# Kernel tuning notes

Measured on AMD Instinct MI355X. Metric: run time of the kernel, lower is better.

Reference implementation:

```python
import jax, jax.numpy as jnp
import numpy as np

K = 2  # kernel_size == stride, padding=0, dilation=1 -> non-overlapping 2x2x2 blocks


def setup_inputs() -> dict:
    key = jax.random.key(0)
    # (b, c, s, w, h) volumetric batch
    x = jax.random.normal(key, (8, 1, 64, 192, 192), dtype=jnp.float32)
    return {"x": x}


def _extract_blocks(x, k):
    # Faithful to extract_patches_3d with stride==kernel, padding=0, dilation=1:
    # the double unfold + permute + flat view yields rows ordered (b, c, do, ho, wo),
    # each row the flattened k*k*k patch.
    b, c, s, w, h = x.shape
    blk = x.reshape(b, c, s // k, k, w // k, k, h // k, k)
    blk = blk.transpose(0, 1, 2, 4, 6, 3, 5, 7)  # (b,c,do,ho,wo,k,k,k)
    return blk.reshape(-1, k * k * k)  # (N, k^3)


def reference(x):
    b, c, s, w, h = x.shape
    data = _extract_blocks(x, K)            # (N, 8)
    mean = jnp.mean(data, axis=0)           # (8,)
    centered = data - mean
    # torch.svd: data = U S V^T ; jax returns vh = V^T
    _, _, vh = jnp.linalg.svd(centered, full_matrices=False)
    pca_components = vh[:1].T               # (8, n_components=1)
    reduced = centered @ pca_components     # (N, 1)
    out = reduced.reshape(b, c, s // K, w // K, h // K)
    return out, mean, pca_components
```

## Files before the change

kernel.cpp:

```cpp
#include <hip/hip_runtime.h>

constexpr int NB     = 8 * 32 * 96 * 96;
constexpr int NQUAD  = NB / 4;
constexpr int NACC   = 44;
constexpr int GRID_A = 768;
constexpr int TPB    = 256;
constexpr int GRID_P = 768;

__global__ __launch_bounds__(TPB, 4)
void reduce_kernel(const float* __restrict__ x, float* __restrict__ partials,
                   unsigned int* __restrict__ ctr, unsigned int* __restrict__ flag) {
  if (blockIdx.x == 0 && threadIdx.x == 0) { *ctr = 0u; *flag = 0u; }

  float acc[NACC];
#pragma unroll
  for (int i = 0; i < NACC; ++i) acc[i] = 0.0f;

  int t = threadIdx.x;
  int tid = blockIdx.x * TPB + t;
  const int stride = GRID_A * TPB;
  for (int q = tid; q < NQUAD; q += stride) {
    int hq = q % 24;
    int t1 = q / 24;
    int wo = t1 % 96;
    int t2 = t1 / 96;
    int so = t2 % 32;
    int b  = t2 / 32;
    const float* base = x + (((b * 64 + 2 * so) * 192 + 2 * wo) * 192 + 8 * hq);
    float4 a0 = *(const float4*)(base);
    float4 b0 = *(const float4*)(base + 4);
    float4 a1 = *(const float4*)(base + 192);
    float4 b1 = *(const float4*)(base + 196);
    float4 a2 = *(const float4*)(base + 192 * 192);
    float4 b2 = *(const float4*)(base + 192 * 192 + 4);
    float4 a3 = *(const float4*)(base + 192 * 192 + 192);
    float4 b3 = *(const float4*)(base + 192 * 192 + 196);
    float P[4][8] = {
      {a0.x, a0.y, a1.x, a1.y, a2.x, a2.y, a3.x, a3.y},
      {a0.z, a0.w, a1.z, a1.w, a2.z, a2.w, a3.z, a3.w},
      {b0.x, b0.y, b1.x, b1.y, b2.x, b2.y, b3.x, b3.y},
      {b0.z, b0.w, b1.z, b1.w, b2.z, b2.w, b3.z, b3.w}};
#pragma unroll
    for (int a = 0; a < 8; ++a)
      acc[a] += (P[0][a] + P[1][a]) + (P[2][a] + P[3][a]);
    int k = 8;
#pragma unroll
    for (int a = 0; a < 8; ++a)
#pragma unroll
      for (int c = a; c < 8; ++c) {
        float tt = P[0][a] * P[0][c];
        tt += P[1][a] * P[1][c];
        tt += P[2][a] * P[2][c];
        tt += P[3][a] * P[3][c];
        acc[k++] += tt;
      }
  }

#pragma unroll
  for (int i = 0; i < NACC; ++i) {
    float v = acc[i];
    for (int off = 32; off >= 1; off >>= 1) v += __shfl_down(v, off, 64);
    acc[i] = v;
  }
  __shared__ float lds[4][NACC];
  int lane = t & 63;
  int wv   = t >> 6;
  if (lane == 0) {
#pragma unroll
    for (int i = 0; i < NACC; ++i) lds[wv][i] = acc[i];
  }
  __syncthreads();
  if (t < NACC) {
    float s = lds[0][t] + lds[1][t] + lds[2][t] + lds[3][t];
    partials[t * GRID_A + blockIdx.x] = s;
  }
}

__device__ __forceinline__ float rdlane(float x, int lane) {
  return __int_as_float(__builtin_amdgcn_readlane(__float_as_int(x), lane));
}

template <int P, int Q>
__device__ __forceinline__ void jrot(const float (&r)[8], float& ct, float& st) {
  float app = rdlane(r[P], P);
  float aqq = rdlane(r[Q], Q);
  float apq = rdlane(r[Q], P);
  float theta = (aqq - app) * 0.5f * __builtin_amdgcn_rcpf(apq);
  float root  = __builtin_amdgcn_sqrtf(theta * theta + 1.0f);
  float tmag  = __builtin_amdgcn_rcpf(fabsf(theta) + root);
  float tt    = copysignf(tmag, theta);
  float c     = __builtin_amdgcn_rsqf(tt * tt + 1.0f);
  float s     = tt * c;
  bool zero   = (apq == 0.0f);
  ct = zero ? 1.0f : c;
  st = zero ? 0.0f : s;
}

template <int P, int Q>
__device__ __forceinline__ void jcol(float (&r)[8], float (&v)[8], float c, float s) {
  float rp = r[P], rq = r[Q];
  r[P] = c * rp - s * rq;
  r[Q] = s * rp + c * rq;
  float vp = v[P], vq = v[Q];
  v[P] = c * vp - s * vq;
  v[Q] = s * vp + c * vq;
}

template <int P0,int Q0,int P1,int Q1,int P2,int Q2,int P3,int Q3>
__device__ __forceinline__ void jacobi_round(float (&r)[8], float (&v)[8], int i) {
  float c0,s0,c1,s1,c2,s2,c3,s3;
  jrot<P0,Q0>(r, c0, s0);
  jrot<P1,Q1>(r, c1, s1);
  jrot<P2,Q2>(r, c2, s2);
  jrot<P3,Q3>(r, c3, s3);
  jcol<P0,Q0>(r, v, c0, s0);
  jcol<P1,Q1>(r, v, c1, s1);
  jcol<P2,Q2>(r, v, c2, s2);
  jcol<P3,Q3>(r, v, c3, s3);
  float alpha = 1.0f, beta = 0.0f;
  int plane = i;
  if (i == P0) { alpha = c0; beta = -s0; plane = Q0; }
  if (i == Q0) { alpha = c0; beta =  s0; plane = P0; }
  if (i == P1) { alpha = c1; beta = -s1; plane = Q1; }
  if (i == Q1) { alpha = c1; beta =  s1; plane = P1; }
  if (i == P2) { alpha = c2; beta = -s2; plane = Q2; }
  if (i == Q2) { alpha = c2; beta =  s2; plane = P2; }
  if (i == P3) { alpha = c3; beta = -s3; plane = Q3; }
  if (i == Q3) { alpha = c3; beta =  s3; plane = P3; }
  float prow[8];
#pragma unroll
  for (int j = 0; j < 8; ++j) prow[j] = __shfl(r[j], plane, 64);
#pragma unroll
  for (int j = 0; j < 8; ++j) r[j] = alpha * r[j] + beta * prow[j];
}

__global__ __launch_bounds__(TPB, 4)
void project_solve_kernel(const float* __restrict__ x,
                          const float* __restrict__ partials,
                          double* __restrict__ sums_d,
                          unsigned int* __restrict__ ctr,
                          unsigned int* __restrict__ flag,
                          float* __restrict__ res,
                          float* __restrict__ out,
                          float* __restrict__ out_tail) {
  int t = threadIdx.x;

  if (blockIdx.x < NACC) {
    double s = 0.0;
    if (t < GRID_A / 4) {
      float4 u = ((const float4*)(partials + blockIdx.x * GRID_A))[t];
      s = (double)u.x + (double)u.y + (double)u.z + (double)u.w;
    }
    for (int off = 32; off >= 1; off >>= 1) s += __shfl_down(s, off, 64);
    __shared__ double ldsd[4];
    __shared__ bool is_last;
    if ((t & 63) == 0) ldsd[t >> 6] = s;
    __syncthreads();
    if (t == 0) {
      sums_d[blockIdx.x] = ldsd[0] + ldsd[1] + ldsd[2] + ldsd[3];
      __threadfence();
      unsigned int old = atomicAdd(ctr, 1u);
      is_last = (old == (unsigned int)(NACC - 1));
    }
    __syncthreads();
    if (is_last) {
      __threadfence();
      __shared__ double sums[NACC];
      if (t < NACC) sums[t] = sums_d[t];
      __syncthreads();
      if (t < 64) {
        const int i = t & 7;
        const double invN = 1.0 / (double)NB;
        double mean[8];
#pragma unroll
        for (int j = 0; j < 8; ++j) mean[j] = sums[j] * invN;
        double mean_i = mean[0];
#pragma unroll
        for (int k = 1; k < 8; ++k) if (i == k) mean_i = mean[k];
        double rowd[8];
#pragma unroll
        for (int j = 0; j < 8; ++j) {
          int p = i < j ? i : j;
          int q = i < j ? j : i;
          int idx = 8 + p * 8 - (p * (p - 1)) / 2 + (q - p);
          rowd[j] = sums[idx] - (double)NB * mean_i * mean[j];
        }
        double tr = 0.0;
#pragma unroll
        for (int k = 0; k < 8; ++k) tr += __shfl(rowd[k], k, 64);
        double shift = tr * 0.125;

        float r[8], v[8];
#pragma unroll
        for (int j = 0; j < 8; ++j) {
          double d = rowd[j] - (j == i ? shift : 0.0);
          r[j] = (float)(d * (1.0 / 1536.0));
          v[j] = (j == i) ? 1.0f : 0.0f;
        }
#pragma unroll 1
        for (int sweep = 0; sweep < 5; ++sweep) {
          jacobi_round<7,0, 1,6, 2,5, 3,4>(r, v, i);
          jacobi_round<7,1, 2,0, 3,6, 4,5>(r, v, i);
          jacobi_round<7,2, 3,1, 4,0, 5,6>(r, v, i);
          jacobi_round<7,3, 4,2, 5,1, 6,0>(r, v, i);
          jacobi_round<7,4, 5,3, 6,2, 0,1>(r, v, i);
          jacobi_round<7,5, 6,4, 0,3, 1,2>(r, v, i);
          jacobi_round<7,6, 0,5, 1,4, 2,3>(r, v, i);
        }
        float diag[8];
#pragma unroll
        for (int k = 0; k < 8; ++k) diag[k] = rdlane(r[k], k);
        int best = 0; float bd = diag[0];
#pragma unroll
        for (int k = 1; k < 8; ++k) if (diag[k] > bd) { bd = diag[k]; best = k; }
        float vi = v[0];
#pragma unroll
        for (int k = 1; k < 8; ++k) if (best == k) vi = v[k];
        float vec[8];
#pragma unroll
        for (int k = 0; k < 8; ++k) vec[k] = rdlane(vi, k);
        float nrm2 = 0.0f;
#pragma unroll
        for (int k = 0; k < 8; ++k) nrm2 += vec[k] * vec[k];
        float inv = 1.0f / sqrtf(nrm2);
#pragma unroll
        for (int k = 0; k < 8; ++k) vec[k] *= inv;
        int m = 0; float am = fabsf(vec[0]);
#pragma unroll
        for (int k = 1; k < 8; ++k) { float aa = fabsf(vec[k]); if (aa > am) { am = aa; m = k; } }
        float vm = vec[0];
#pragma unroll
        for (int k = 1; k < 8; ++k) if (m == k) vm = vec[k];
        if (vm > 0.0f) {
#pragma unroll
          for (int k = 0; k < 8; ++k) vec[k] = -vec[k];
        }
        double c0d = 0.0;
#pragma unroll
        for (int k = 0; k < 8; ++k) c0d += mean[k] * (double)vec[k];
        float mi = (float)mean[0];
#pragma unroll
        for (int k = 1; k < 8; ++k) if (i == k) mi = (float)mean[k];
        float vl = vec[0];
#pragma unroll
        for (int k = 1; k < 8; ++k) if (i == k) vl = vec[k];
        if (t < 8) {
          res[t]          = vl;
          out_tail[t]     = mi;
          out_tail[8 + t] = vl;
        }
        if (t == 0) res[8] = (float)c0d;
      }
      __syncthreads();
      if (t == 0) {
        __threadfence();
        __hip_atomic_store(flag, 1u, __ATOMIC_RELEASE, __HIP_MEMORY_SCOPE_AGENT);
      }
    }
  }

  __shared__ float s_res[9];
  if (t == 0) {
    while (__hip_atomic_load(flag, __ATOMIC_RELAXED, __HIP_MEMORY_SCOPE_AGENT) == 0u)
      __builtin_amdgcn_s_sleep(8);
  }
  __syncthreads();
  if (t < 9)
    s_res[t] = __hip_atomic_load(&res[t], __ATOMIC_RELAXED, __HIP_MEMORY_SCOPE_AGENT);
  __syncthreads();

  float w0 = s_res[0], w1 = s_res[1], w2 = s_res[2], w3 = s_res[3];
  float w4 = s_res[4], w5 = s_res[5], w6 = s_res[6], w7 = s_res[7];
  float c0 = s_res[8];
  float4* out4 = (float4*)out;
  const int stride = GRID_P * TPB;
  for (int q = blockIdx.x * TPB + t; q < NQUAD; q += stride) {
    int hq = q % 24;
    int t1 = q / 24;
    int wo = t1 % 96;
    int t2 = t1 / 96;
    int so = t2 % 32;
    int b  = t2 / 32;
    const float* base = x + (((b * 64 + 2 * so) * 192 + 2 * wo) * 192 + 8 * hq);
    float4 a0 = *(const float4*)(base);
    float4 b0 = *(const float4*)(base + 4);
    float4 a1 = *(const float4*)(base + 192);
    float4 b1 = *(const float4*)(base + 196);
    float4 a2 = *(const float4*)(base + 192 * 192);
    float4 b2 = *(const float4*)(base + 192 * 192 + 4);
    float4 a3 = *(const float4*)(base + 192 * 192 + 192);
    float4 b3 = *(const float4*)(base + 192 * 192 + 196);
    float o0 = a0.x * w0 + a0.y * w1 + a1.x * w2 + a1.y * w3
             + a2.x * w4 + a2.y * w5 + a3.x * w6 + a3.y * w7 - c0;
    float o1 = a0.z * w0 + a0.w * w1 + a1.z * w2 + a1.w * w3
             + a2.z * w4 + a2.w * w5 + a3.z * w6 + a3.w * w7 - c0;
    float o2 = b0.x * w0 + b0.y * w1 + b1.x * w2 + b1.y * w3
             + b2.x * w4 + b2.y * w5 + b3.x * w6 + b3.y * w7 - c0;
    float o3 = b0.z * w0 + b0.w * w1 + b1.z * w2 + b1.w * w3
             + b2.z * w4 + b2.w * w5 + b3.z * w6 + b3.w * w7 - c0;
    out4[q] = make_float4(o0, o1, o2, o3);
  }
}

extern "C" void kernel_launch(void* const* d_in, const int* in_sizes, int n_in,
                              void* d_out, int out_size, void* d_ws, size_t ws_size,
                              hipStream_t stream) {
  (void)in_sizes; (void)n_in; (void)out_size; (void)ws_size;
  const float* x = (const float*)d_in[0];
  float* out = (float*)d_out;
  float* partials   = (float*)d_ws;
  double* sums_d    = (double*)(partials + NACC * GRID_A);
  float* res        = (float*)(sums_d + NACC);
  unsigned int* ctr = (unsigned int*)(res + 16);
  unsigned int* flg = ctr + 1;

  reduce_kernel<<<GRID_A, TPB, 0, stream>>>(x, partials, ctr, flg);
  project_solve_kernel<<<GRID_P, TPB, 0, stream>>>(x, partials, sums_d, ctr, flg,
                                                   res, out, out + NB);
}
```

Before: 55.26 us.

## Move final partial reduction into reduce kernel, solve eigenproblem redundantly per block

Removes the spin-wait flag handshake in the projection kernel. The last 44 blocks of the reduce kernel now wait on an atomic counter and each folds one accumulator row into sums_d. Every projection block then recomputes the 8x8 Jacobi eigen-solve locally, so no cross-block dependency remains. Also fixes the grid-stride loops at three iterations and adds a memset launch to reset the counter. Trades redundant per-block solve work and a small extra memset for the removal of the serialized global wait.

Measured after the change: 116.7 us. 2.11x slower.

```diff
diff --git a/kernel.cpp b/kernel.cpp
--- a/kernel.cpp
+++ b/kernel.cpp
@@ -6,20 +6,20 @@
 constexpr int GRID_A = 768;
 constexpr int TPB    = 256;
 constexpr int GRID_P = 768;
+constexpr int STRIDE = GRID_A * TPB;
 
 __global__ __launch_bounds__(TPB, 4)
 void reduce_kernel(const float* __restrict__ x, float* __restrict__ partials,
-                   unsigned int* __restrict__ ctr, unsigned int* __restrict__ flag) {
-  if (blockIdx.x == 0 && threadIdx.x == 0) { *ctr = 0u; *flag = 0u; }
-
+                   double* __restrict__ sums_d, unsigned int* __restrict__ ctr) {
   float acc[NACC];
 #pragma unroll
   for (int i = 0; i < NACC; ++i) acc[i] = 0.0f;
 
   int t = threadIdx.x;
   int tid = blockIdx.x * TPB + t;
-  const int stride = GRID_A * TPB;
-  for (int q = tid; q < NQUAD; q += stride) {
+#pragma unroll
+  for (int it = 0; it < 3; ++it) {
+    int q = tid + it * STRIDE;
     int hq = q % 24;
     int t1 = q / 24;
     int wo = t1 % 96;
@@ -74,6 +74,34 @@
     float s = lds[0][t] + lds[1][t] + lds[2][t] + lds[3][t];
     partials[t * GRID_A + blockIdx.x] = s;
   }
+
+  __threadfence();
+  __syncthreads();
+  __shared__ unsigned int oldv;
+  if (t == 0) oldv = atomicAdd(ctr, 1u);
+  __syncthreads();
+  unsigned int old = oldv;
+  if (old < (unsigned int)(GRID_A - NACC)) return;
+  int row = (int)old - (GRID_A - NACC);
+
+  if (t == 0) {
+    while (__hip_atomic_load(ctr, __ATOMIC_RELAXED, __HIP_MEMORY_SCOPE_AGENT)
+           < (unsigned int)GRID_A)
+      __builtin_amdgcn_s_sleep(1);
+  }
+  __syncthreads();
+  __threadfence();
+
+  double s = 0.0;
+  if (t < GRID_A / 4) {
+    float4 u = ((const float4*)(partials + row * GRID_A))[t];
+    s = (double)u.x + (double)u.y + (double)u.z + (double)u.w;
+  }
+  for (int off = 32; off >= 1; off >>= 1) s += __shfl_down(s, off, 64);
+  __shared__ double ldsd[4];
+  if (lane == 0) ldsd[wv] = s;
+  __syncthreads();
+  if (t == 0) sums_d[row] = ldsd[0] + ldsd[1] + ldsd[2] + ldsd[3];
 }
 
 __device__ __forceinline__ float rdlane(float x, int lane) {
@@ -136,145 +164,112 @@
 
 __global__ __launch_bounds__(TPB, 4)
 void project_solve_kernel(const float* __restrict__ x,
-                          const float* __restrict__ partials,
-                          double* __restrict__ sums_d,
-                          unsigned int* __restrict__ ctr,
-                          unsigned int* __restrict__ flag,
-                          float* __restrict__ res,
+                          const double* __restrict__ sums_d,
                           float* __restrict__ out,
                           float* __restrict__ out_tail) {
+  __shared__ double sums[NACC];
+  __shared__ float s_res[9];
   int t = threadIdx.x;
 
-  if (blockIdx.x < NACC) {
-    double s = 0.0;
-    if (t < GRID_A / 4) {
-      float4 u = ((const float4*)(partials + blockIdx.x * GRID_A))[t];
-      s = (double)u.x + (double)u.y + (double)u.z + (double)u.w;
-    }
-    for (int off = 32; off >= 1; off >>= 1) s += __shfl_down(s, off, 64);
-    __shared__ double ldsd[4];
-    __shared__ bool is_last;
-    if ((t & 63) == 0) ldsd[t >> 6] = s;
-    __syncthreads();
-    if (t == 0) {
-      sums_d[blockIdx.x] = ldsd[0] + ldsd[1] + ldsd[2] + ldsd[3];
-      __threadfence();
-      unsigned int old = atomicAdd(ctr, 1u);
-      is_last = (old == (unsigned int)(NACC - 1));
-    }
-    __syncthreads();
-    if (is_last) {
-      __threadfence();
-      __shared__ double sums[NACC];
-      if (t < NACC) sums[t] = sums_d[t];
-      __syncthreads();
-      if (t < 64) {
-        const int i = t & 7;
-        const double invN = 1.0 / (double)NB;
-        double mean[8];
-#pragma unroll
-        for (int j = 0; j < 8; ++j) mean[j] = sums[j] * invN;
-        double mean_i = mean[0];
-#pragma unroll
-        for (int k = 1; k < 8; ++k) if (i == k) mean_i = mean[k];
-        double rowd[8];
-#pragma unroll
-        for (int j = 0; j < 8; ++j) {
-          int p = i < j ? i : j;
-          int q = i < j ? j : i;
-          int idx = 8 + p * 8 - (p * (p - 1)) / 2 + (q - p);
-          rowd[j] = sums[idx] - (double)NB * mean_i * mean[j];
-        }
-        double tr = 0.0;
-#pragma unroll
-        for (int k = 0; k < 8; ++k) tr += __shfl(rowd[k], k, 64);
-        double shift = tr * 0.125;
-
-        float r[8], v[8];
-#pragma unroll
-        for (int j = 0; j < 8; ++j) {
-          double d = rowd[j] - (j == i ? shift : 0.0);
-          r[j] = (float)(d * (1.0 / 1536.0));
-          v[j] = (j == i) ? 1.0f : 0.0f;
-        }
+  if (t < NACC) sums[t] = sums_d[t];
+  __syncthreads();
+
+  if (t < 64) {
+    const int i = t & 7;
+    const double invN = 1.0 / (double)NB;
+    double mean[8];
+#pragma unroll
+    for (int j = 0; j < 8; ++j) mean[j] = sums[j] * invN;
+    double mean_i = mean[0];
+#pragma unroll
+    for (int k = 1; k < 8; ++k) if (i == k) mean_i = mean[k];
+    double rowd[8];
+#pragma unroll
+    for (int j = 0; j < 8; ++j) {
+      int p = i < j ? i : j;
+      int q = i < j ? j : i;
+      int idx = 8 + p * 8 - (p * (p - 1)) / 2 + (q - p);
+      rowd[j] = sums[idx] - (double)NB * mean_i * mean[j];
+    }
+    double tr = 0.0;
+#pragma unroll
+    for (int k = 0; k < 8; ++k) tr += __shfl(rowd[k], k, 64);
+    double shift = tr * 0.125;
+
+    float r[8], v[8];
+#pragma unroll
+    for (int j = 0; j < 8; ++j) {
+      double d = rowd[j] - (j == i ? shift : 0.0);
+      r[j] = (float)(d * (1.0 / 1536.0));
+      v[j] = (j == i) ? 1.0f : 0.0f;
+    }
 #pragma unroll 1
-        for (int sweep = 0; sweep < 5; ++sweep) {
-          jacobi_round<7,0, 1,6, 2,5, 3,4>(r, v, i);
-          jacobi_round<7,1, 2,0, 3,6, 4,5>(r, v, i);
-          jacobi_round<7,2, 3,1, 4,0, 5,6>(r, v, i);
-          jacobi_round<7,3, 4,2, 5,1, 6,0>(r, v, i);
-          jacobi_round<7,4, 5,3, 6,2, 0,1>(r, v, i);
-          jacobi_round<7,5, 6,4, 0,3, 1,2>(r, v, i);
-          jacobi_round<7,6, 0,5, 1,4, 2,3>(r, v, i);
-        }
-        float diag[8];
-#pragma unroll
-        for (int k = 0; k < 8; ++k) diag[k] = rdlane(r[k], k);
-        int best = 0; float bd = diag[0];
-#pragma unroll
-        for (int k = 1; k < 8; ++k) if (diag[k] > bd) { bd = diag[k]; best = k; }
-        float vi = v[0];
-#pragma unroll
-        for (int k = 1; k < 8; ++k) if (best == k) vi = v[k];
-        float vec[8];
-#pragma unroll
-        for (int k = 0; k < 8; ++k) vec[k] = rdlane(vi, k);
-        float nrm2 = 0.0f;
-#pragma unroll
-        for (int k = 0; k < 8; ++k) nrm2 += vec[k] * vec[k];
-        float inv = 1.0f / sqrtf(nrm2);
-#pragma unroll
-        for (int k = 0; k < 8; ++k) vec[k] *= inv;
-        int m = 0; float am = fabsf(vec[0]);
-#pragma unroll
-        for (int k = 1; k < 8; ++k) { float aa = fabsf(vec[k]); if (aa > am) { am = aa; m = k; } }
-        float vm = vec[0];
-#pragma unroll
-        for (int k = 1; k < 8; ++k) if (m == k) vm = vec[k];
-        if (vm > 0.0f) {
-#pragma unroll
-          for (int k = 0; k < 8; ++k) vec[k] = -vec[k];
-        }
-        double c0d = 0.0;
-#pragma unroll
-        for (int k = 0; k < 8; ++k) c0d += mean[k] * (double)vec[k];
-        float mi = (float)mean[0];
-#pragma unroll
-        for (int k = 1; k < 8; ++k) if (i == k) mi = (float)mean[k];
-        float vl = vec[0];
-#pragma unroll
-        for (int k = 1; k < 8; ++k) if (i == k) vl = vec[k];
-        if (t < 8) {
-          res[t]          = vl;
-          out_tail[t]     = mi;
-          out_tail[8 + t] = vl;
-        }
-        if (t == 0) res[8] = (float)c0d;
+    for (int sweep = 0; sweep < 5; ++sweep) {
+      jacobi_round<7,0, 1,6, 2,5, 3,4>(r, v, i);
+      jacobi_round<7,1, 2,0, 3,6, 4,5>(r, v, i);
+      jacobi_round<7,2, 3,1, 4,0, 5,6>(r, v, i);
+      jacobi_round<7,3, 4,2, 5,1, 6,0>(r, v, i);
+      jacobi_round<7,4, 5,3, 6,2, 0,1>(r, v, i);
+      jacobi_round<7,5, 6,4, 0,3, 1,2>(r, v, i);
+      jacobi_round<7,6, 0,5, 1,4, 2,3>(r, v, i);
+    }
+    float diag[8];
+#pragma unroll
+    for (int k = 0; k < 8; ++k) diag[k] = rdlane(r[k], k);
+    int best = 0; float bd = diag[0];
+#pragma unroll
+    for (int k = 1; k < 8; ++k) if (diag[k] > bd) { bd = diag[k]; best = k; }
+    float vi = v[0];
+#pragma unroll
+    for (int k = 1; k < 8; ++k) if (best == k) vi = v[k];
+    float vec[8];
+#pragma unroll
+    for (int k = 0; k < 8; ++k) vec[k] = rdlane(vi, k);
+    float nrm2 = 0.0f;
+#pragma unroll
+    for (int k = 0; k < 8; ++k) nrm2 += vec[k] * vec[k];
+    float inv = 1.0f / sqrtf(nrm2);
+#pragma unroll
+    for (int k = 0; k < 8; ++k) vec[k] *= inv;
+    int m = 0; float am = fabsf(vec[0]);
+#pragma unroll
+    for (int k = 1; k < 8; ++k) { float aa = fabsf(vec[k]); if (aa > am) { am = aa; m = k; } }
+    float vm = vec[0];
+#pragma unroll
+    for (int k = 1; k < 8; ++k) if (m == k) vm = vec[k];
+    if (vm > 0.0f) {
+#pragma unroll
+      for (int k = 0; k < 8; ++k) vec[k] = -vec[k];
+    }
+    double c0d = 0.0;
+#pragma unroll
+    for (int k = 0; k < 8; ++k) c0d += mean[k] * (double)vec[k];
+    float mi = (float)mean[0];
+#pragma unroll
+    for (int k = 1; k < 8; ++k) if (i == k) mi = (float)mean[k];
+    float vl = vec[0];
+#pragma unroll
+    for (int k = 1; k < 8; ++k) if (i == k) vl = vec[k];
+
+    if (t < 8) {
+      s_res[t] = vl;
+      if (blockIdx.x == 0) {
+        out_tail[t]     = mi;
+        out_tail[8 + t] = vl;
       }
-      __syncthreads();
-      if (t == 0) {
-        __threadfence();
-        __hip_atomic_store(flag, 1u, __ATOMIC_RELEASE, __HIP_MEMORY_SCOPE_AGENT);
-      }
-    }
-  }
-
-  __shared__ float s_res[9];
-  if (t == 0) {
-    while (__hip_atomic_load(flag, __ATOMIC_RELAXED, __HIP_MEMORY_SCOPE_AGENT) == 0u)
-      __builtin_amdgcn_s_sleep(8);
-  }
-  __syncthreads();
-  if (t < 9)
-    s_res[t] = __hip_atomic_load(&res[t], __ATOMIC_RELAXED, __HIP_MEMORY_SCOPE_AGENT);
+    }
+    if (t == 0) s_res[8] = (float)c0d;
+  }
   __syncthreads();
 
   float w0 = s_res[0], w1 = s_res[1], w2 = s_res[2], w3 = s_res[3];
   float w4 = s_res[4], w5 = s_res[5], w6 = s_res[6], w7 = s_res[7];
   float c0 = s_res[8];
   float4* out4 = (float4*)out;
-  const int stride = GRID_P * TPB;
-  for (int q = blockIdx.x * TPB + t; q < NQUAD; q += stride) {
+  int tid = blockIdx.x * TPB + t;
+#pragma unroll
+  for (int it = 0; it < 3; ++it) {
+    int q = tid + it * STRIDE;
     int hq = q % 24;
     int t1 = q / 24;
     int wo = t1 % 96;
@@ -310,11 +305,9 @@
   float* out = (float*)d_out;
   float* partials   = (float*)d_ws;
   double* sums_d    = (double*)(partials + NACC * GRID_A);
-  float* res        = (float*)(sums_d + NACC);
-  unsigned int* ctr = (unsigned int*)(res + 16);
-  unsigned int* flg = ctr + 1;
-
-  reduce_kernel<<<GRID_A, TPB, 0, stream>>>(x, partials, ctr, flg);
-  project_solve_kernel<<<GRID_P, TPB, 0, stream>>>(x, partials, sums_d, ctr, flg,
-                                                   res, out, out + NB);
-}
+  unsigned int* ctr = (unsigned int*)(sums_d + NACC);
+
+  hipMemsetAsync((void*)ctr, 0, sizeof(unsigned int), stream);
+  reduce_kernel<<<GRID_A, TPB, 0, stream>>>(x, partials, sums_d, ctr);
+  project_solve_kernel<<<GRID_P, TPB, 0, stream>>>(x, sums_d, out, out + NB);
+}
```
